# Performance work log

Hardware: AMD Instinct MI355X
Metric: run time of the kernel (lower is better)

Reference implementation:

```python
import jax, jax.numpy as jnp
import numpy as np

EMBED_DIM = 1024
NUM_HEADS = 16
HEAD_DIM = EMBED_DIM // NUM_HEADS


def setup_inputs() -> dict:
    key = jax.random.key(0)
    ks = jax.random.split(key, 9)
    B, T, C = 2, 2048, EMBED_DIM
    s = 1.0 / np.sqrt(C)
    inp = {
        "x": jax.random.normal(ks[0], (B, T, C), dtype=jnp.float32),
        "Wq": jax.random.uniform(ks[1], (C, C), jnp.float32, -s, s),
        "bq": jax.random.uniform(ks[2], (C,), jnp.float32, -s, s),
        "Wk": jax.random.uniform(ks[3], (C, C), jnp.float32, -s, s),
        "bk": jax.random.uniform(ks[4], (C,), jnp.float32, -s, s),
        "Wv": jax.random.uniform(ks[5], (C, C), jnp.float32, -s, s),
        "bv": jax.random.uniform(ks[6], (C,), jnp.float32, -s, s),
        "Wo": jax.random.uniform(ks[7], (C, C), jnp.float32, -s, s),
        "bo": jax.random.uniform(ks[8], (C,), jnp.float32, -s, s),
    }
    return inp


def reference(x, Wq, bq, Wk, bk, Wv, bv, Wo, bo):
    B, T, C = x.shape
    H, D = NUM_HEADS, HEAD_DIM

    def heads(W, b):
        # [B,T,C] -> [B,H,T,D]
        return (x @ W + b).reshape(B, T, H, D).transpose(0, 2, 1, 3)

    q = heads(Wq, bq)
    k = heads(Wk, bk)
    v = heads(Wv, bv)

    scores = jnp.einsum('bhtd,bhsd->bhts', q, k) / np.sqrt(D).astype(np.float32)
    causal = jnp.tril(jnp.ones((T, T), dtype=bool))  # [T,T]
    scores = jnp.where(causal[None, None], scores, -jnp.inf)
    weights = jax.nn.softmax(scores, axis=-1)
    out = jnp.einsum('bhts,bhsd->bhtd', weights, v)  # [B,H,T,D]
    out = out.transpose(0, 2, 1, 3).reshape(B, T, C)
    return out @ Wo + bo
```

## Files before the change

### kernel.cpp

```cpp
#include <hip/hip_runtime.h>
#include <stdint.h>

#define T_LEN 2048
#define C_DIM 1024
#define NHEAD 16
#define HDIM  64
#define MTOT  4096

typedef __bf16 bf16;
typedef __bf16 bf16x4 __attribute__((ext_vector_type(4)));
typedef __bf16 bf16x8 __attribute__((ext_vector_type(8)));
typedef float  f32x4  __attribute__((ext_vector_type(4)));

__device__ __forceinline__ bf16 f2bf(float f) {
    union { float f; unsigned u; } x; x.f = f;
    unsigned r = x.u + 0x7fffu + ((x.u >> 16) & 1u);
    unsigned short h = (unsigned short)(r >> 16);
    return __builtin_bit_cast(bf16, h);
}

__device__ __forceinline__ void g2l16(const void* g, const void* l) {
    __builtin_amdgcn_global_load_lds(
        (const __attribute__((address_space(1))) unsigned int*)(uintptr_t)g,
        (__attribute__((address_space(3))) unsigned int*)(uint32_t)(uintptr_t)l,
        16, 0, 0);
}


__global__ void cast_x_kernel(const float* __restrict__ x, bf16* __restrict__ xb) {
    int f = blockIdx.x * 256 + threadIdx.x;
    const float4* p = (const float4*)x + (size_t)f * 2;
    float4 a = p[0], b = p[1];
    bf16x8 o;
    o[0] = f2bf(a.x); o[1] = f2bf(a.y); o[2] = f2bf(a.z); o[3] = f2bf(a.w);
    o[4] = f2bf(b.x); o[5] = f2bf(b.y); o[6] = f2bf(b.z); o[7] = f2bf(b.w);
    ((bf16x8*)xb)[f] = o;
}

__global__ void cast_w_kernel(const float* __restrict__ W0, const float* __restrict__ W1,
                              const float* __restrict__ W2, const float* __restrict__ W3,
                              bf16* __restrict__ wt) {
    __shared__ float tile[64][68];
    const int tid = threadIdx.x;
    const int w = blockIdx.z;
    const float* W = (w == 0) ? W0 : (w == 1) ? W1 : (w == 2) ? W2 : W3;
    const int kb = blockIdx.x * 64, nb = blockIdx.y * 64;
#pragma unroll
    for (int pass = 0; pass < 4; ++pass) {
        int row = pass * 16 + (tid >> 4);
        int col = (tid & 15) * 4;
        float4 v = *(const float4*)(W + (size_t)(kb + row) * 1024 + nb + col);
        *(float4*)(&tile[row][col]) = v;
    }
    __syncthreads();
#pragma unroll
    for (int pass = 0; pass < 2; ++pass) {
        int s = pass * 256 + tid;
        int nn = s >> 3, c = s & 7;
        bf16x8 o;
#pragma unroll
        for (int j = 0; j < 8; ++j) o[j] = f2bf(tile[c * 8 + j][nn]);
        *(bf16x8*)(wt + (size_t)w * 1048576 + (size_t)(nb + nn) * 1024 + kb + c * 8) = o;
    }
}

__global__ void transpose_v_kernel(const bf16* __restrict__ V, bf16* __restrict__ Vtp) {
    __shared__ bf16 tile[128][72];
    const int tid = threadIdx.x;
    const int t0 = blockIdx.x * 128, bh = blockIdx.y;
    const size_t hb = (size_t)bh * 131072;
#pragma unroll
    for (int pass = 0; pass < 4; ++pass) {
        int s = pass * 256 + tid;
        int row = s >> 3, c = s & 7;
        bf16x8 v = *(const bf16x8*)(V + hb + (size_t)(t0 + row) * 64 + c * 8);
        *(bf16x8*)(&tile[row][c * 8]) = v;
    }
    __syncthreads();
#pragma unroll
    for (int pass = 0; pass < 4; ++pass) {
        int s = pass * 256 + tid;
        int d = s >> 4, ch = s & 15;
        bf16x8 o;
#pragma unroll
        for (int j = 0; j < 8; ++j) {
            int orig = 32 * (ch >> 2) + 16 * (j >> 2) + 4 * (ch & 3) + (j & 3);
            o[j] = tile[orig][d];
        }
        *(bf16x8*)(Vtp + hb + (size_t)d * 2048 + t0 + ch * 8) = o;
    }
}

__global__ __launch_bounds__(256, 2)
void gemm_bt_kernel(const bf16* __restrict__ A, const bf16* __restrict__ WtAll,
                    const float* __restrict__ b0, const float* __restrict__ b1,
                    const float* __restrict__ b2, bf16* __restrict__ outQKV) {
    __shared__ char lds[32768];
    bf16* As = (bf16*)lds;
    bf16* Bs = (bf16*)(lds + 16384);

    const int tid = threadIdx.x;
    const int lane = tid & 63, wid = tid >> 6;
    const int r = lane & 15, q4 = lane >> 4;
    const int mbase = blockIdx.y * 128;
    const int nbase = blockIdx.x * 128;
    const int z = blockIdx.z;
    const bf16* Bt = WtAll + (size_t)z * 1048576;
    const float* bias = (z == 0) ? b0 : (z == 1) ? b1 : b2;
    const float osc = (z == 0) ? 0.125f : 1.0f;

    const int wm = (wid >> 1) * 64;
    const int wn = (wid & 1) * 64;

    float bv[4];
#pragma unroll
    for (int j = 0; j < 4; ++j) bv[j] = bias[nbase + wn + j * 16 + r];

    f32x4 acc[4][4];
#pragma unroll
    for (int i = 0; i < 4; ++i)
#pragma unroll
        for (int j = 0; j < 4; ++j) acc[i][j] = f32x4{0.f, 0.f, 0.f, 0.f};

    for (int kt = 0; kt < 16; ++kt) {
        int kb = kt * 64;
#pragma unroll
        for (int p = 0; p < 4; ++p) {
            int s = p * 256 + tid;
            int row = s >> 3, blk = s & 7;
            int sb = blk ^ (row & 7);
            g2l16(A  + (size_t)(mbase + row) * 1024 + kb + sb * 8, (char*)As + s * 16);
            g2l16(Bt + (size_t)(nbase + row) * 1024 + kb + sb * 8, (char*)Bs + s * 16);
        }
        __syncthreads();
#pragma unroll
        for (int ks = 0; ks < 2; ++ks) {
            int blk = ks * 4 + q4;
            bf16x8 a[4], b[4];
#pragma unroll
            for (int i = 0; i < 4; ++i) {
                int rowa = wm + i * 16 + r;
                a[i] = *(const bf16x8*)((const char*)As + rowa * 128 + ((blk ^ (rowa & 7)) * 16));
                int rowb = wn + i * 16 + r;
                b[i] = *(const bf16x8*)((const char*)Bs + rowb * 128 + ((blk ^ (rowb & 7)) * 16));
            }
#pragma unroll
            for (int i = 0; i < 4; ++i)
#pragma unroll
                for (int j = 0; j < 4; ++j)
                    acc[i][j] = __builtin_amdgcn_mfma_f32_16x16x32_bf16(a[i], b[j], acc[i][j], 0, 0, 0);
        }
        __syncthreads();
    }

#pragma unroll
    for (int i = 0; i < 4; ++i) {
        int m0 = mbase + wm + i * 16 + q4 * 4;
#pragma unroll
        for (int j = 0; j < 4; ++j) {
            int n = nbase + wn + j * 16 + r;
#pragma unroll
            for (int reg = 0; reg < 4; ++reg) {
                float v = (acc[i][j][reg] + bv[j]) * osc;
                int mm = m0 + reg;
                int bi = mm >> 11, t = mm & 2047, h = n >> 6, d = n & 63;
                outQKV[(size_t)z * 4194304 + ((size_t)(bi * 16 + h) * 2048 + t) * 64 + d] = f2bf(v);
            }
        }
    }
}

__global__ __launch_bounds__(256, 2)
void gemm_o_kernel(const bf16* __restrict__ A, const bf16* __restrict__ Bt,
                   const float* __restrict__ bias, float* __restrict__ out) {
    __shared__ char lds[24576];
    bf16* As = (bf16*)lds;
    bf16* Bs = (bf16*)(lds + 16384);

    const int tid = threadIdx.x;
    const int lane = tid & 63, wid = tid >> 6;
    const int r = lane & 15, q4 = lane >> 4;
    const int nb = blockIdx.x * 64;
    const int mb = blockIdx.y * 128;
    const int wm = (wid >> 1) * 64;
    const int wn = (wid & 1) * 32;

    float bv[2];
#pragma unroll
    for (int j = 0; j < 2; ++j) bv[j] = bias[nb + wn + j * 16 + r];

    f32x4 acc[4][2];
#pragma unroll
    for (int i = 0; i < 4; ++i)
#pragma unroll
        for (int j = 0; j < 2; ++j) acc[i][j] = f32x4{0.f, 0.f, 0.f, 0.f};

    for (int kt = 0; kt < 16; ++kt) {
        int kb = kt * 64;
#pragma unroll
        for (int p = 0; p < 4; ++p) {
            int s = p * 256 + tid;
            int row = s >> 3, blk = s & 7;
            g2l16(A + (size_t)(mb + row) * 1024 + kb + ((blk ^ (row & 7)) * 8), (char*)As + s * 16);
        }
#pragma unroll
        for (int p = 0; p < 2; ++p) {
            int s = p * 256 + tid;
            int row = s >> 3, blk = s & 7;
            g2l16(Bt + (size_t)(nb + row) * 1024 + kb + ((blk ^ (row & 7)) * 8), (char*)Bs + s * 16);
        }
        __syncthreads();
#pragma unroll
        for (int ks = 0; ks < 2; ++ks) {
            int blk = ks * 4 + q4;
            bf16x8 a[4], b[2];
#pragma unroll
            for (int i = 0; i < 4; ++i) {
                int rowa = wm + i * 16 + r;
                a[i] = *(const bf16x8*)((const char*)As + rowa * 128 + ((blk ^ (rowa & 7)) * 16));
            }
#pragma unroll
            for (int j = 0; j < 2; ++j) {
                int rowb = wn + j * 16 + r;
                b[j] = *(const bf16x8*)((const char*)Bs + rowb * 128 + ((blk ^ (rowb & 7)) * 16));
            }
#pragma unroll
            for (int i = 0; i < 4; ++i)
#pragma unroll
                for (int j = 0; j < 2; ++j)
                    acc[i][j] = __builtin_amdgcn_mfma_f32_16x16x32_bf16(a[i], b[j], acc[i][j], 0, 0, 0);
        }
        __syncthreads();
    }

#pragma unroll
    for (int i = 0; i < 4; ++i) {
        int m0 = mb + wm + i * 16 + q4 * 4;
#pragma unroll
        for (int j = 0; j < 2; ++j) {
            int n = nb + wn + j * 16 + r;
#pragma unroll
            for (int reg = 0; reg < 4; ++reg)
                out[(size_t)(m0 + reg) * 1024 + n] = acc[i][j][reg] + bv[j];
        }
    }
}

__global__ __launch_bounds__(256, 1)
void attn_kernel(const bf16* __restrict__ Q, const bf16* __restrict__ K,
                 const bf16* __restrict__ Vtp, bf16* __restrict__ Aout) {
    __shared__ char lds[65536];

    const int tid = threadIdx.x, lane = tid & 63, wid = tid >> 6;
    const int r = lane & 15, q4 = lane >> 4;
    const int p = blockIdx.x >> 5;
    const int bh = blockIdx.x & 31;
    const int b = bh >> 4, h = bh & 15;
    const size_t hb = (size_t)bh * 131072;

    const int qiA = p, qiB = 15 - p;
    const int itB0 = qiA + 1;
    const int ittot = itB0 + qiB + 1;

    bf16x8 qf[2][2], qfB[2][2];
#pragma unroll
    for (int i = 0; i < 2; ++i)
#pragma unroll
        for (int ks = 0; ks < 2; ++ks) {
            int rA = qiA * 128 + wid * 32 + i * 16 + r;
            int rB = qiB * 128 + wid * 32 + i * 16 + r;
            qf[i][ks]  = *(const bf16x8*)(Q + hb + (size_t)rA * 64 + ks * 32 + q4 * 8);
            qfB[i][ks] = *(const bf16x8*)(Q + hb + (size_t)rB * 64 + ks * 32 + q4 * 8);
        }

    f32x4 o[2][4];
    float lip[2];
#pragma unroll
    for (int i = 0; i < 2; ++i) {
        lip[i] = 0.f;
#pragma unroll
        for (int jd = 0; jd < 4; ++jd) o[i][jd] = f32x4{0.f, 0.f, 0.f, 0.f};
    }

    auto stage = [&](int buf, int kb) {
        char* Kb = lds + buf * 16384;
        char* Vb = lds + 32768 + buf * 16384;
#pragma unroll
        for (int pp = 0; pp < 4; ++pp) {
            int s = pp * 256 + tid;
            int row = s >> 3, blk = s & 7;
            g2l16(K + hb + (size_t)(kb + row) * 64 + ((blk ^ (row & 7)) * 8), Kb + s * 16);
        }
#pragma unroll
        for (int pp = 0; pp < 4; ++pp) {
            int s = pp * 256 + tid;
            int row = s >> 4, ch = s & 15;
            g2l16(Vtp + hb + (size_t)row * 2048 + kb + ((ch ^ (row & 15)) * 8), Vb + s * 16);
        }
    };

    auto epilogue = [&](int qbase) {
#pragma unroll
        for (int i = 0; i < 2; ++i) {
            float li = lip[i];
            li += __shfl_xor(li, 16);
            li += __shfl_xor(li, 32);
            float inv = 1.f / li;
            int q = qbase + wid * 32 + i * 16 + r;
#pragma unroll
            for (int dsub = 0; dsub < 4; ++dsub) {
                bf16x4 w;
#pragma unroll
                for (int reg = 0; reg < 4; ++reg) w[reg] = f2bf(o[i][dsub][reg] * inv);
                *(bf16x4*)(Aout + ((size_t)(b * 2048 + q)) * 1024 + h * 64 + dsub * 16 + q4 * 4) = w;
            }
        }
    };

    stage(0, 0);

    for (int it = 0; it < ittot; ++it) {
        __syncthreads();
        const int cb = it & 1;
        if (it + 1 < ittot) {
            int nit = it + 1;
            int nkt = (nit < itB0) ? nit : (nit - itB0);
            stage(nit & 1, nkt * 128);
        }
        if (it == itB0) {
            epilogue(qiA * 128);
#pragma unroll
            for (int i = 0; i < 2; ++i) {
                lip[i] = 0.f;
#pragma unroll
                for (int jd = 0; jd < 4; ++jd) o[i][jd] = f32x4{0.f, 0.f, 0.f, 0.f};
#pragma unroll
                for (int ks = 0; ks < 2; ++ks) qf[i][ks] = qfB[i][ks];
            }
        }
        const bool inB = (it >= itB0);
        const int qi = inB ? qiB : qiA;
        const int kt = inB ? (it - itB0) : it;
        const int kb = kt * 128;
        const int qbase = qi * 128;
        const char* Kb = lds + cb * 16384;
        const char* Vb = lds + 32768 + cb * 16384;

        f32x4 sc[2][8];
#pragma unroll
        for (int st = 0; st < 8; ++st) {
            int rowk = st * 16 + r;
            bf16x8 ak0 = *(const bf16x8*)(Kb + rowk * 128 + ((q4 ^ (rowk & 7)) * 16));
            bf16x8 ak1 = *(const bf16x8*)(Kb + rowk * 128 + (((4 + q4) ^ (rowk & 7)) * 16));
#pragma unroll
            for (int i = 0; i < 2; ++i) {
                sc[i][st] = __builtin_amdgcn_mfma_f32_16x16x32_bf16(ak0, qf[i][0], f32x4{0.f, 0.f, 0.f, 0.f}, 0, 0, 0);
                sc[i][st] = __builtin_amdgcn_mfma_f32_16x16x32_bf16(ak1, qf[i][1], sc[i][st], 0, 0, 0);
            }
        }

        const bool lastt = (kt == qi);
        bf16x8 pb[2][4];
#pragma unroll
        for (int i = 0; i < 2; ++i) {
            int qrow = qbase + wid * 32 + i * 16 + r;
#pragma unroll
            for (int c = 0; c < 4; ++c) {
                bf16x8 t;
                if (lastt) {
#pragma unroll
                    for (int j = 0; j < 8; ++j) {
                        int st = 2 * c + (j >> 2), reg = j & 3;
                        int key = kb + st * 16 + q4 * 4 + reg;
                        float sv = (key > qrow) ? -1e30f : sc[i][st][reg];
                        float pv = __expf(sv);
                        lip[i] += pv;
                        t[j] = (bf16)pv;
                    }
                } else {
#pragma unroll
                    for (int j = 0; j < 8; ++j) {
                        int st = 2 * c + (j >> 2), reg = j & 3;
                        float pv = __expf(sc[i][st][reg]);
                        lip[i] += pv;
                        t[j] = (bf16)pv;
                    }
                }
                pb[i][c] = t;
            }
        }

#pragma unroll
        for (int c = 0; c < 4; ++c) {
            int sidx = c * 4 + q4;
#pragma unroll
            for (int dsub = 0; dsub < 4; ++dsub) {
                int rowd = dsub * 16 + r;
                bf16x8 av = *(const bf16x8*)(Vb + rowd * 256 + ((sidx ^ (rowd & 15)) * 16));
                o[0][dsub] = __builtin_amdgcn_mfma_f32_16x16x32_bf16(av, pb[0][c], o[0][dsub], 0, 0, 0);
                o[1][dsub] = __builtin_amdgcn_mfma_f32_16x16x32_bf16(av, pb[1][c], o[1][dsub], 0, 0, 0);
            }
        }
    }

    epilogue(qiB * 128);
}


extern "C" void kernel_launch(void* const* d_in, const int* in_sizes, int n_in,
                              void* d_out, int out_size, void* d_ws, size_t ws_size,
                              hipStream_t stream) {
    const float* x  = (const float*)d_in[0];
    const float* Wq = (const float*)d_in[1];
    const float* bq = (const float*)d_in[2];
    const float* Wk = (const float*)d_in[3];
    const float* bk = (const float*)d_in[4];
    const float* Wv = (const float*)d_in[5];
    const float* bv = (const float*)d_in[6];
    const float* Wo = (const float*)d_in[7];
    const float* bo = (const float*)d_in[8];
    float* out = (float*)d_out;

    char* ws = (char*)d_ws;
    bf16* xb   = (bf16*)(ws);
    bf16* wt   = (bf16*)(ws + 8388608);
    bf16* qkv  = (bf16*)(ws + 16777216);
    bf16* vtp  = (bf16*)(ws + 41943040);
    bf16* attn = (bf16*)(ws + 50331648);

    hipLaunchKernelGGL(cast_x_kernel, dim3(2048), dim3(256), 0, stream, x, xb);
    hipLaunchKernelGGL(cast_w_kernel, dim3(16, 16, 4), dim3(256), 0, stream, Wq, Wk, Wv, Wo, wt);
    hipLaunchKernelGGL(gemm_bt_kernel, dim3(8, 32, 3), dim3(256), 0, stream,
                       xb, wt, bq, bk, bv, qkv);
    hipLaunchKernelGGL(transpose_v_kernel, dim3(16, 32), dim3(256), 0, stream,
                       qkv + (size_t)2 * 4194304, vtp);
    hipLaunchKernelGGL(attn_kernel, dim3(256), dim3(256), 0, stream,
                       qkv, qkv + 4194304, vtp, attn);
    hipLaunchKernelGGL(gemm_o_kernel, dim3(16, 32), dim3(256), 0, stream,
                       attn, wt + (size_t)3 * 1048576, bo, out);
}
```

Baseline: 180.9 us.

## Run both attention query tiles concurrently with 512 threads, using MFMA row sums and exp2

The attention kernel now uses 512 threads per block. Each wave owns 16 rows of both paired query tiles and processes them together in one shared key loop, so K/V staging is no longer repeated in two sequential phases. Softmax row sums are computed with an MFMA against a ones vector instead of a scalar accumulation plus shuffles, and exp2 replaces exp, with log2(e) folded into the Q scale. The two projection GEMMs swap MFMA operand order so each lane holds four consecutive columns, which allows vectorised bias loads and bf16x4/float4 stores. The trade-offs are higher register pressure at 512 threads, extra MFMAs for the row sums, and idle waves in the short tile once its causal range ends.

```diff
diff --git a/kernel.cpp b/kernel.cpp
--- a/kernel.cpp
+++ b/kernel.cpp
@@ -107,14 +107,14 @@
     const int z = blockIdx.z;
     const bf16* Bt = WtAll + (size_t)z * 1048576;
     const float* bias = (z == 0) ? b0 : (z == 1) ? b1 : b2;
-    const float osc = (z == 0) ? 0.125f : 1.0f;
+    const float osc = (z == 0) ? 0.18033688011112042f : 1.0f;
 
     const int wm = (wid >> 1) * 64;
     const int wn = (wid & 1) * 64;
 
-    float bv[4];
-#pragma unroll
-    for (int j = 0; j < 4; ++j) bv[j] = bias[nbase + wn + j * 16 + r];
+    float4 bvv[4];
+#pragma unroll
+    for (int j = 0; j < 4; ++j) bvv[j] = *(const float4*)(bias + nbase + wn + j * 16 + q4 * 4);
 
     f32x4 acc[4][4];
 #pragma unroll
@@ -148,24 +148,25 @@
             for (int i = 0; i < 4; ++i)
 #pragma unroll
                 for (int j = 0; j < 4; ++j)
-                    acc[i][j] = __builtin_amdgcn_mfma_f32_16x16x32_bf16(a[i], b[j], acc[i][j], 0, 0, 0);
+                    acc[i][j] = __builtin_amdgcn_mfma_f32_16x16x32_bf16(b[j], a[i], acc[i][j], 0, 0, 0);
         }
         __syncthreads();
     }
 
 #pragma unroll
     for (int i = 0; i < 4; ++i) {
-        int m0 = mbase + wm + i * 16 + q4 * 4;
+        int m = mbase + wm + i * 16 + r;
+        int bi = m >> 11, t = m & 2047;
 #pragma unroll
         for (int j = 0; j < 4; ++j) {
-            int n = nbase + wn + j * 16 + r;
-#pragma unroll
-            for (int reg = 0; reg < 4; ++reg) {
-                float v = (acc[i][j][reg] + bv[j]) * osc;
-                int mm = m0 + reg;
-                int bi = mm >> 11, t = mm & 2047, h = n >> 6, d = n & 63;
-                outQKV[(size_t)z * 4194304 + ((size_t)(bi * 16 + h) * 2048 + t) * 64 + d] = f2bf(v);
-            }
+            int n0 = nbase + wn + j * 16 + q4 * 4;
+            bf16x4 w;
+            w[0] = f2bf((acc[i][j][0] + bvv[j].x) * osc);
+            w[1] = f2bf((acc[i][j][1] + bvv[j].y) * osc);
+            w[2] = f2bf((acc[i][j][2] + bvv[j].z) * osc);
+            w[3] = f2bf((acc[i][j][3] + bvv[j].w) * osc);
+            int h = n0 >> 6, d = n0 & 63;
+            *(bf16x4*)(outQKV + (size_t)z * 4194304 + ((size_t)(bi * 16 + h) * 2048 + t) * 64 + d) = w;
         }
     }
 }
@@ -185,9 +186,9 @@
     const int wm = (wid >> 1) * 64;
     const int wn = (wid & 1) * 32;
 
-    float bv[2];
-#pragma unroll
-    for (int j = 0; j < 2; ++j) bv[j] = bias[nb + wn + j * 16 + r];
+    float4 bvv[2];
+#pragma unroll
+    for (int j = 0; j < 2; ++j) bvv[j] = *(const float4*)(bias + nb + wn + j * 16 + q4 * 4);
 
     f32x4 acc[4][2];
 #pragma unroll
@@ -228,25 +229,28 @@
             for (int i = 0; i < 4; ++i)
 #pragma unroll
                 for (int j = 0; j < 2; ++j)
-                    acc[i][j] = __builtin_amdgcn_mfma_f32_16x16x32_bf16(a[i], b[j], acc[i][j], 0, 0, 0);
+                    acc[i][j] = __builtin_amdgcn_mfma_f32_16x16x32_bf16(b[j], a[i], acc[i][j], 0, 0, 0);
         }
         __syncthreads();
     }
 
 #pragma unroll
     for (int i = 0; i < 4; ++i) {
-        int m0 = mb + wm + i * 16 + q4 * 4;
+        int m = mb + wm + i * 16 + r;
 #pragma unroll
         for (int j = 0; j < 2; ++j) {
-            int n = nb + wn + j * 16 + r;
-#pragma unroll
-            for (int reg = 0; reg < 4; ++reg)
-                out[(size_t)(m0 + reg) * 1024 + n] = acc[i][j][reg] + bv[j];
-        }
-    }
-}
-
-__global__ __launch_bounds__(256, 1)
+            int n0 = nb + wn + j * 16 + q4 * 4;
+            float4 w;
+            w.x = acc[i][j][0] + bvv[j].x;
+            w.y = acc[i][j][1] + bvv[j].y;
+            w.z = acc[i][j][2] + bvv[j].z;
+            w.w = acc[i][j][3] + bvv[j].w;
+            *(float4*)(out + (size_t)m * 1024 + n0) = w;
+        }
+    }
+}
+
+__global__ __launch_bounds__(512, 2)
 void attn_kernel(const bf16* __restrict__ Q, const bf16* __restrict__ K,
                  const bf16* __restrict__ Vtp, bf16* __restrict__ Aout) {
     __shared__ char lds[65536];
@@ -258,26 +262,27 @@
     const int b = bh >> 4, h = bh & 15;
     const size_t hb = (size_t)bh * 131072;
 
-    const int qiA = p, qiB = 15 - p;
-    const int itB0 = qiA + 1;
-    const int ittot = itB0 + qiB + 1;
-
-    bf16x8 qf[2][2], qfB[2][2];
+    const int qi[2] = { p, 15 - p };
+    const int ittot = 16 - p;
+
+    bf16x8 qf[2][2];
 #pragma unroll
     for (int i = 0; i < 2; ++i)
 #pragma unroll
         for (int ks = 0; ks < 2; ++ks) {
-            int rA = qiA * 128 + wid * 32 + i * 16 + r;
-            int rB = qiB * 128 + wid * 32 + i * 16 + r;
-            qf[i][ks]  = *(const bf16x8*)(Q + hb + (size_t)rA * 64 + ks * 32 + q4 * 8);
-            qfB[i][ks] = *(const bf16x8*)(Q + hb + (size_t)rB * 64 + ks * 32 + q4 * 8);
-        }
+            int row = qi[i] * 128 + wid * 16 + r;
+            qf[i][ks] = *(const bf16x8*)(Q + hb + (size_t)row * 64 + ks * 32 + q4 * 8);
+        }
+
+    bf16x8 ones;
+#pragma unroll
+    for (int j = 0; j < 8; ++j) ones[j] = (bf16)1.0f;
 
     f32x4 o[2][4];
-    float lip[2];
+    f32x4 osum[2];
 #pragma unroll
     for (int i = 0; i < 2; ++i) {
-        lip[i] = 0.f;
+        osum[i] = f32x4{0.f, 0.f, 0.f, 0.f};
 #pragma unroll
         for (int jd = 0; jd < 4; ++jd) o[i][jd] = f32x4{0.f, 0.f, 0.f, 0.f};
     }
@@ -286,34 +291,16 @@
         char* Kb = lds + buf * 16384;
         char* Vb = lds + 32768 + buf * 16384;
 #pragma unroll
-        for (int pp = 0; pp < 4; ++pp) {
-            int s = pp * 256 + tid;
+        for (int pp = 0; pp < 2; ++pp) {
+            int s = pp * 512 + tid;
             int row = s >> 3, blk = s & 7;
             g2l16(K + hb + (size_t)(kb + row) * 64 + ((blk ^ (row & 7)) * 8), Kb + s * 16);
         }
 #pragma unroll
-        for (int pp = 0; pp < 4; ++pp) {
-            int s = pp * 256 + tid;
+        for (int pp = 0; pp < 2; ++pp) {
+            int s = pp * 512 + tid;
             int row = s >> 4, ch = s & 15;
             g2l16(Vtp + hb + (size_t)row * 2048 + kb + ((ch ^ (row & 15)) * 8), Vb + s * 16);
-        }
-    };
-
-    auto epilogue = [&](int qbase) {
-#pragma unroll
-        for (int i = 0; i < 2; ++i) {
-            float li = lip[i];
-            li += __shfl_xor(li, 16);
-            li += __shfl_xor(li, 32);
-            float inv = 1.f / li;
-            int q = qbase + wid * 32 + i * 16 + r;
-#pragma unroll
-            for (int dsub = 0; dsub < 4; ++dsub) {
-                bf16x4 w;
-#pragma unroll
-                for (int reg = 0; reg < 4; ++reg) w[reg] = f2bf(o[i][dsub][reg] * inv);
-                *(bf16x4*)(Aout + ((size_t)(b * 2048 + q)) * 1024 + h * 64 + dsub * 16 + q4 * 4) = w;
-            }
         }
     };
 
@@ -322,29 +309,11 @@
     for (int it = 0; it < ittot; ++it) {
         __syncthreads();
         const int cb = it & 1;
-        if (it + 1 < ittot) {
-            int nit = it + 1;
-            int nkt = (nit < itB0) ? nit : (nit - itB0);
-            stage(nit & 1, nkt * 128);
-        }
-        if (it == itB0) {
-            epilogue(qiA * 128);
-#pragma unroll
-            for (int i = 0; i < 2; ++i) {
-                lip[i] = 0.f;
-#pragma unroll
-                for (int jd = 0; jd < 4; ++jd) o[i][jd] = f32x4{0.f, 0.f, 0.f, 0.f};
-#pragma unroll
-                for (int ks = 0; ks < 2; ++ks) qf[i][ks] = qfB[i][ks];
-            }
-        }
-        const bool inB = (it >= itB0);
-        const int qi = inB ? qiB : qiA;
-        const int kt = inB ? (it - itB0) : it;
-        const int kb = kt * 128;
-        const int qbase = qi * 128;
+        if (it + 1 < ittot) stage((it + 1) & 1, (it + 1) * 128);
+        const int kb = it * 128;
         const char* Kb = lds + cb * 16384;
         const char* Vb = lds + 32768 + cb * 16384;
+        const bool aAct = (it <= qi[0]);
 
         f32x4 sc[2][8];
 #pragma unroll
@@ -352,58 +321,66 @@
             int rowk = st * 16 + r;
             bf16x8 ak0 = *(const bf16x8*)(Kb + rowk * 128 + ((q4 ^ (rowk & 7)) * 16));
             bf16x8 ak1 = *(const bf16x8*)(Kb + rowk * 128 + (((4 + q4) ^ (rowk & 7)) * 16));
-#pragma unroll
-            for (int i = 0; i < 2; ++i) {
-                sc[i][st] = __builtin_amdgcn_mfma_f32_16x16x32_bf16(ak0, qf[i][0], f32x4{0.f, 0.f, 0.f, 0.f}, 0, 0, 0);
-                sc[i][st] = __builtin_amdgcn_mfma_f32_16x16x32_bf16(ak1, qf[i][1], sc[i][st], 0, 0, 0);
-            }
-        }
-
-        const bool lastt = (kt == qi);
-        bf16x8 pb[2][4];
+            sc[1][st] = __builtin_amdgcn_mfma_f32_16x16x32_bf16(ak0, qf[1][0], f32x4{0.f, 0.f, 0.f, 0.f}, 0, 0, 0);
+            sc[1][st] = __builtin_amdgcn_mfma_f32_16x16x32_bf16(ak1, qf[1][1], sc[1][st], 0, 0, 0);
+            if (aAct) {
+                sc[0][st] = __builtin_amdgcn_mfma_f32_16x16x32_bf16(ak0, qf[0][0], f32x4{0.f, 0.f, 0.f, 0.f}, 0, 0, 0);
+                sc[0][st] = __builtin_amdgcn_mfma_f32_16x16x32_bf16(ak1, qf[0][1], sc[0][st], 0, 0, 0);
+            }
+        }
+
 #pragma unroll
         for (int i = 0; i < 2; ++i) {
-            int qrow = qbase + wid * 32 + i * 16 + r;
+            if (i == 0 && !aAct) continue;
+            const bool dia = (it == qi[i]);
+            int qrow = qi[i] * 128 + wid * 16 + r;
+            bf16x8 pb[4];
 #pragma unroll
             for (int c = 0; c < 4; ++c) {
                 bf16x8 t;
-                if (lastt) {
+                if (dia) {
 #pragma unroll
                     for (int j = 0; j < 8; ++j) {
                         int st = 2 * c + (j >> 2), reg = j & 3;
                         int key = kb + st * 16 + q4 * 4 + reg;
                         float sv = (key > qrow) ? -1e30f : sc[i][st][reg];
-                        float pv = __expf(sv);
-                        lip[i] += pv;
-                        t[j] = (bf16)pv;
+                        t[j] = (bf16)__builtin_amdgcn_exp2f(sv);
                     }
                 } else {
 #pragma unroll
                     for (int j = 0; j < 8; ++j) {
                         int st = 2 * c + (j >> 2), reg = j & 3;
-                        float pv = __expf(sc[i][st][reg]);
-                        lip[i] += pv;
-                        t[j] = (bf16)pv;
+                        t[j] = (bf16)__builtin_amdgcn_exp2f(sc[i][st][reg]);
                     }
                 }
-                pb[i][c] = t;
-            }
-        }
-
-#pragma unroll
-        for (int c = 0; c < 4; ++c) {
-            int sidx = c * 4 + q4;
-#pragma unroll
-            for (int dsub = 0; dsub < 4; ++dsub) {
-                int rowd = dsub * 16 + r;
-                bf16x8 av = *(const bf16x8*)(Vb + rowd * 256 + ((sidx ^ (rowd & 15)) * 16));
-                o[0][dsub] = __builtin_amdgcn_mfma_f32_16x16x32_bf16(av, pb[0][c], o[0][dsub], 0, 0, 0);
-                o[1][dsub] = __builtin_amdgcn_mfma_f32_16x16x32_bf16(av, pb[1][c], o[1][dsub], 0, 0, 0);
-            }
-        }
-    }
-
-    epilogue(qiB * 128);
+                pb[c] = t;
+            }
+#pragma unroll
+            for (int c = 0; c < 4; ++c) {
+                int sidx = c * 4 + q4;
+                osum[i] = __builtin_amdgcn_mfma_f32_16x16x32_bf16(ones, pb[c], osum[i], 0, 0, 0);
+#pragma unroll
+                for (int dsub = 0; dsub < 4; ++dsub) {
+                    int rowd = dsub * 16 + r;
+                    bf16x8 av = *(const bf16x8*)(Vb + rowd * 256 + ((sidx ^ (rowd & 15)) * 16));
+                    o[i][dsub] = __builtin_amdgcn_mfma_f32_16x16x32_bf16(av, pb[c], o[i][dsub], 0, 0, 0);
+                }
+            }
+        }
+    }
+
+#pragma unroll
+    for (int i = 0; i < 2; ++i) {
+        float inv = 1.f / osum[i][0];
+        int q = qi[i] * 128 + wid * 16 + r;
+#pragma unroll
+        for (int dsub = 0; dsub < 4; ++dsub) {
+            bf16x4 w;
+#pragma unroll
+            for (int reg = 0; reg < 4; ++reg) w[reg] = f2bf(o[i][dsub][reg] * inv);
+            *(bf16x4*)(Aout + ((size_t)(b * 2048 + q)) * 1024 + h * 64 + dsub * 16 + q4 * 4) = w;
+        }
+    }
 }
 
 
@@ -434,7 +411,7 @@
                        xb, wt, bq, bk, bv, qkv);
     hipLaunchKernelGGL(transpose_v_kernel, dim3(16, 32), dim3(256), 0, stream,
                        qkv + (size_t)2 * 4194304, vtp);
-    hipLaunchKernelGGL(attn_kernel, dim3(256), dim3(256), 0, stream,
+    hipLaunchKernelGGL(attn_kernel, dim3(256), dim3(512), 0, stream,
                        qkv, qkv + 4194304, vtp, attn);
     hipLaunchKernelGGL(gemm_o_kernel, dim3(16, 32), dim3(256), 0, stream,
                        attn, wt + (size_t)3 * 1048576, bo, out);
```

Result: faster. 176.8 us (-2.3%).
